# Performance work log

Hardware: AMD Instinct MI355X
Metric: run time of the kernel (lower is better)

The kernel has to match this reference:

```python
import jax, jax.numpy as jnp
import numpy as np

B, TQ, N, E, K = 256, 64, 196, 1024, 512


def setup_inputs() -> dict:
    key = jax.random.key(0)
    ks = jax.random.split(key, 12)
    s_e = 1.0 / np.sqrt(E)
    s_k = 1.0 / np.sqrt(K)
    return {
        "ques_feat": jax.random.normal(ks[0], (B, TQ, E), jnp.float32),
        "img_feat": jax.random.normal(ks[1], (B, E, N), jnp.float32),
        "mask": jnp.ones((B, TQ), jnp.float32),
        # img_corr_dim: Linear(E, E)
        "Wc": jax.random.normal(ks[2], (E, E), jnp.float32) * s_e,
        "bc": jnp.zeros((E,), jnp.float32),
        # ques_embed_dim: Linear(E, K)
        "Wq": jax.random.normal(ks[3], (E, K), jnp.float32) * s_e,
        "bq": jnp.zeros((K,), jnp.float32),
        # img_embed_dim: Linear(E, K)
        "Wi": jax.random.normal(ks[4], (E, K), jnp.float32) * s_e,
        "bi": jnp.zeros((K,), jnp.float32),
        # ques_atten_embedding: Linear(K, 1)
        "wqa": jax.random.normal(ks[5], (K,), jnp.float32) * s_k,
        "bqa": jnp.zeros((), jnp.float32),
        # img_atten_embedding: Linear(K, 1)
        "wia": jax.random.normal(ks[6], (K,), jnp.float32) * s_k,
        "bia": jnp.zeros((), jnp.float32),
    }


def reference(ques_feat, img_feat, mask, Wc, bc, Wq, bq, Wi, bi, wqa, bqa, wia, bia):
    # img_feat: [B, E, N] -> work in [B, N, E] layout
    img_t = jnp.swapaxes(img_feat, 1, 2)                      # [B, N, E]
    img_corr = img_t @ Wc + bc                                # [B, N, E]
    # affinity matrix: tanh(Q @ C^T) -> [B, Tq, N]
    weight = jnp.tanh(jnp.einsum("bqe,bne->bqn", ques_feat, img_corr))
    ques_embed = ques_feat @ Wq + bq                          # [B, Tq, K]
    img_embed = img_t @ Wi + bi                               # [B, N, K]
    # image attention branch
    transform_ques = jnp.einsum("bqk,bqn->bnk", ques_embed, weight)  # [B, N, K]
    img_h = jnp.tanh(transform_ques + img_embed)              # [B, N, K] (dropout p=0)
    img_score = img_h @ wia + bia                             # [B, N]
    img_atten = jax.nn.softmax(img_score, axis=-1)            # [B, N]
    # question attention branch
    transform_img = jnp.einsum("bnk,bqn->bqk", img_embed, weight)    # [B, Tq, K]
    ques_h = jnp.tanh(transform_img + ques_embed)             # [B, Tq, K]
    ques_score = (ques_h @ wqa + bqa) * mask                  # [B, Tq]
    ques_atten = jax.nn.softmax(ques_score, axis=-1)          # [B, Tq]
    # attended features
    ques_atten_feat = jnp.einsum("bq,bqe->be", ques_atten, ques_feat)  # [B, E]
    img_atten_feat = jnp.einsum("bn,bne->be", img_atten, img_t)        # [B, E]
    return ques_atten_feat, img_atten_feat
```

## Files before the change

kernel.cpp:

```cpp
#include <hip/hip_runtime.h>
#include <math.h>


typedef float f32x4 __attribute__((ext_vector_type(4)));
typedef short bf16x8 __attribute__((ext_vector_type(8)));
typedef unsigned short u16;

__device__ __forceinline__ float fast_tanh(float x) {
    float ax = fabsf(x);
    float e  = __expf(-2.0f * ax);
    float r  = (1.0f - e) / (1.0f + e);
    return copysignf(r, x);
}
__device__ __forceinline__ u16 f2bf(float f) {
    unsigned u = __float_as_uint(f);
    u += 0x7FFF + ((u >> 16) & 1);
    return (u16)(u >> 16);
}
__device__ __forceinline__ void split_hl(float f, u16 &h, u16 &l) {
    h = f2bf(f);
    float fh = __uint_as_float((unsigned)h << 16);
    l = f2bf(f - fh);
}
__device__ __forceinline__ void gload_lds16(const u16* g, u16* l) {
    __builtin_amdgcn_global_load_lds(
        (const __attribute__((address_space(1))) unsigned int*)(const void*)g,
        (__attribute__((address_space(3))) unsigned int*)(void*)l, 16, 0, 0);
}

__global__ __launch_bounds__(256) void transpose_split_kernel(
    const float* __restrict__ in, u16* __restrict__ oh, u16* __restrict__ ol,
    const int R, const int C, const long inB, const long outB)
{
    __shared__ float tile[64][65];
    const int t = threadIdx.x;
    const int c0 = blockIdx.x * 64;
    const int r0 = blockIdx.y * 64;
    const long bz = blockIdx.z;
    const float* ib = in + bz * inB;

    #pragma unroll
    for (int i = 0; i < 16; ++i) {
        int idx = i * 256 + t;
        int rl = idx >> 6, cl = idx & 63;
        float v = 0.f;
        if (c0 + cl < C) v = ib[(size_t)(r0 + rl) * C + c0 + cl];
        tile[rl][cl] = v;
    }
    __syncthreads();
    #pragma unroll
    for (int i = 0; i < 16; ++i) {
        int idx = i * 256 + t;
        int cl = idx >> 6, rl = idx & 63;
        if (c0 + cl < C) {
            float v = tile[rl][cl];
            u16 h, l;
            split_hl(v, h, l);
            size_t o = bz * outB + (size_t)(c0 + cl) * R + r0 + rl;
            oh[o] = h; ol[o] = l;
        }
    }
}

__global__ __launch_bounds__(256) void split_flat_kernel(
    const float* __restrict__ in, u16* __restrict__ oh, u16* __restrict__ ol,
    const int n4)
{
    for (int i = blockIdx.x * 256 + threadIdx.x; i < n4; i += gridDim.x * 256) {
        float4 v = ((const float4*)in)[i];
        u16 h0,h1,h2,h3, l0,l1,l2,l3;
        split_hl(v.x,h0,l0); split_hl(v.y,h1,l1);
        split_hl(v.z,h2,l2); split_hl(v.w,h3,l3);
        ((ushort4*)oh)[i] = make_ushort4(h0,h1,h2,h3);
        ((ushort4*)ol)[i] = make_ushort4(l0,l1,l2,l3);
    }
}

template<int WM, int WN, int OUTMODE, bool BATCHED>
__global__ __launch_bounds__(WM*WN*64) void bf_gemm(
    const u16* __restrict__ Ah, const u16* __restrict__ Al,
    const u16* __restrict__ Bh, const u16* __restrict__ Bl,
    const float* __restrict__ bias,
    float* __restrict__ Cf, u16* __restrict__ Ch, u16* __restrict__ Cl,
    const int M, const int N, const int K,
    const int aB, const int bB, const long cB, const int ldc)
{
    constexpr int NW = WM * WN;
    constexpr int AP = WM * 4;
    constexpr int BP = WN * 4;
    constexpr int TOT = (AP + BP) * 2;
    __shared__ __align__(16) u16 smem[(AP + BP) * 2 * 512];

    const int t  = threadIdx.x;
    const int wid = t >> 6, l = t & 63;
    const int wm = wid / WN, wn = wid % WN;
    const int n0 = blockIdx.x * (WN * 64);
    const int m0 = blockIdx.y * (WM * 64);
    const int bz = BATCHED ? blockIdx.z : 0;

    f32x4 acc[4][4];
    #pragma unroll
    for (int p = 0; p < 4; ++p)
        #pragma unroll
        for (int q = 0; q < 4; ++q)
            acc[p][q] = (f32x4){0.f, 0.f, 0.f, 0.f};

    const int lk = (l >> 4) << 3;
    const int lr = l & 15;

    for (int k0 = 0; k0 < K; k0 += 32) {
        #pragma unroll
        for (int j = wid; j < TOT; j += NW) {
            if (j < 2 * AP) {
                int plane = j / AP, p = j % AP;
                int gm = m0 + p * 16 + lr; gm = min(gm, M - 1);
                const u16* src = plane ? Al : Ah;
                const u16* g = src + (BATCHED ? (size_t)bz * aB : 0)
                             + (size_t)gm * K + k0 + lk;
                gload_lds16(g, smem + (plane * AP + p) * 512);
            } else {
                int jj = j - 2 * AP;
                int plane = jj / BP, p = jj % BP;
                int gn = n0 + p * 16 + lr; gn = min(gn, N - 1);
                const u16* src = plane ? Bl : Bh;
                const u16* g = src + (BATCHED ? (size_t)bz * bB : 0)
                             + (size_t)gn * K + k0 + lk;
                gload_lds16(g, smem + (2 * AP + plane * BP + p) * 512);
            }
        }
        __syncthreads();

        bf16x8 a_h[4], a_l[4], b_h[4], b_l[4];
        #pragma unroll
        for (int p = 0; p < 4; ++p) {
            const u16* pa = smem + (wm * 4 + p) * 512 + l * 8;
            a_h[p] = *(const bf16x8*)pa;
            a_l[p] = *(const bf16x8*)(pa + AP * 512);
        }
        #pragma unroll
        for (int q = 0; q < 4; ++q) {
            const u16* pb = smem + (2 * AP + wn * 4 + q) * 512 + l * 8;
            b_h[q] = *(const bf16x8*)pb;
            b_l[q] = *(const bf16x8*)(pb + BP * 512);
        }
        #pragma unroll
        for (int p = 0; p < 4; ++p)
            #pragma unroll
            for (int q = 0; q < 4; ++q)
                acc[p][q] = __builtin_amdgcn_mfma_f32_16x16x32_bf16(a_h[p], b_h[q], acc[p][q], 0, 0, 0);
        #pragma unroll
        for (int p = 0; p < 4; ++p)
            #pragma unroll
            for (int q = 0; q < 4; ++q)
                acc[p][q] = __builtin_amdgcn_mfma_f32_16x16x32_bf16(a_h[p], b_l[q], acc[p][q], 0, 0, 0);
        #pragma unroll
        for (int p = 0; p < 4; ++p)
            #pragma unroll
            for (int q = 0; q < 4; ++q)
                acc[p][q] = __builtin_amdgcn_mfma_f32_16x16x32_bf16(a_l[p], b_h[q], acc[p][q], 0, 0, 0);
        __syncthreads();
    }

    const int colp = l & 15;
    const int rquad = (l >> 4) * 4;
    #pragma unroll
    for (int q = 0; q < 4; ++q) {
        int col = n0 + wn * 64 + q * 16 + colp;
        if (col >= N) continue;
        float bv = bias ? bias[col] : 0.f;
        #pragma unroll
        for (int p = 0; p < 4; ++p) {
            #pragma unroll
            for (int i = 0; i < 4; ++i) {
                int row = m0 + wm * 64 + p * 16 + rquad + i;
                if (row >= M) continue;
                float v = acc[p][q][i] + bv;
                size_t ci = (BATCHED ? (size_t)bz * cB : 0) + (size_t)row * ldc + col;
                if (OUTMODE == 0) {
                    Cf[ci] = v;
                } else if (OUTMODE == 1) {
                    Cf[ci] = fast_tanh(v);
                } else {
                    u16 h, lo2;
                    split_hl(v, h, lo2);
                    Ch[ci] = h; Cl[ci] = lo2;
                }
            }
        }
    }
}

template<int BM,int BN,int BK,int TM,int TN,int ALOAD,int BLOAD,int NBF,int ACT,bool BATCHED>
__global__ __launch_bounds__(256) void gemm_k(
    const float* __restrict__ A, const float* __restrict__ Bm,
    const float* __restrict__ bias, const float* __restrict__ Dadd,
    float* __restrict__ C,
    const int M, const int Nn, const int K,
    const int ab, const int am, const int ak,
    const int bb, const int bk, const int bn,
    const int cb, const int cm)
{
    static_assert(BK == 16, "staging math assumes BK==16");
    __shared__ __align__(16) float As[BK][BM + 4];
    __shared__ __align__(16) float Bs[BK][BN + 4];

    const int t  = threadIdx.x;
    const int n0 = blockIdx.x * BN;
    const int m0 = blockIdx.y * BM;
    const int bz = BATCHED ? blockIdx.z : 0;
    const int w  = t >> 6;
    const int l  = t & 63;
    const int tx = l & 7, ty = l >> 3;
    const int mloc = (w >> 1) * (BM / 2) + ty * TM;
    const int nloc = (w & 1)  * (BN / 2) + tx * TN;

    float acc[TM][TN];
    #pragma unroll
    for (int i = 0; i < TM; ++i)
        #pragma unroll
        for (int j = 0; j < TN; ++j) acc[i][j] = 0.f;

    for (int k0 = 0; k0 < K; k0 += BK) {
        if (ALOAD == 0) {
            constexpr int NF4 = (BM * BK) / (4 * 256);
            #pragma unroll
            for (int i = 0; i < NF4; ++i) {
                int f4i = i * 256 + t;
                int row = f4i >> 2;
                int kq  = (f4i & 3) << 2;
                int gm = m0 + row, gk = k0 + kq;
                float4 v = make_float4(0.f, 0.f, 0.f, 0.f);
                if (gm < M) {
                    int br, r;
                    if (BATCHED)      { br = bz; r = gm; }
                    else if (NBF > 0) { br = gm / NBF; r = gm - br * NBF; }
                    else              { br = 0;  r = gm; }
                    const float* p = A + (size_t)br * ab + (size_t)r * am + gk;
                    if (gk + 4 <= K) v = *(const float4*)p;
                    else {
                        float tv[4] = {0.f, 0.f, 0.f, 0.f};
                        #pragma unroll
                        for (int j = 0; j < 4; ++j) if (gk + j < K) tv[j] = p[j];
                        v = make_float4(tv[0], tv[1], tv[2], tv[3]);
                    }
                }
                As[kq + 0][row] = v.x; As[kq + 1][row] = v.y;
                As[kq + 2][row] = v.z; As[kq + 3][row] = v.w;
            }
        } else {
            constexpr int NF4 = (BM * BK) / (4 * 256);
            #pragma unroll
            for (int i = 0; i < NF4; ++i) {
                int f4i = i * 256 + t;
                int m4 = f4i % (BM / 4);
                int kk = f4i / (BM / 4);
                int gm = m0 + m4 * 4, gk = k0 + kk;
                float4 v = make_float4(0.f, 0.f, 0.f, 0.f);
                if (gm < M && gk < K) {
                    int br, r;
                    if (BATCHED)      { br = bz; r = gm; }
                    else if (NBF > 0) { br = gm / NBF; r = gm - br * NBF; }
                    else              { br = 0;  r = gm; }
                    const float* p = A + (size_t)br * ab + (size_t)r + (size_t)gk * ak;
                    v = *(const float4*)p;
                }
                *(float4*)&As[kk][m4 * 4] = v;
            }
        }
        if (BLOAD == 0) {
            constexpr int NF4 = (BK * BN) / (4 * 256);
            #pragma unroll
            for (int i = 0; i < NF4; ++i) {
                int f4i = i * 256 + t;
                int nq2 = f4i % (BN / 4);
                int kk = f4i / (BN / 4);
                int gn = n0 + nq2 * 4, gk = k0 + kk;
                float4 v = make_float4(0.f, 0.f, 0.f, 0.f);
                if (gk < K && gn + 4 <= Nn) {
                    const float* p = Bm + (size_t)bz * bb + (size_t)gk * bk + gn;
                    v = *(const float4*)p;
                }
                *(float4*)&Bs[kk][nq2 * 4] = v;
            }
        } else {
            constexpr int NF4 = (BK * BN) / (4 * 256);
            #pragma unroll
            for (int i = 0; i < NF4; ++i) {
                int f4i = i * 256 + t;
                int col = f4i >> 2;
                int kq  = (f4i & 3) << 2;
                int gn = n0 + col, gk = k0 + kq;
                float4 v = make_float4(0.f, 0.f, 0.f, 0.f);
                if (gn < Nn) {
                    const float* p = Bm + (size_t)bz * bb + (size_t)gn * bn + gk;
                    if (gk + 4 <= K) v = *(const float4*)p;
                    else {
                        float tv[4] = {0.f, 0.f, 0.f, 0.f};
                        #pragma unroll
                        for (int j = 0; j < 4; ++j) if (gk + j < K) tv[j] = p[j];
                        v = make_float4(tv[0], tv[1], tv[2], tv[3]);
                    }
                }
                Bs[kq + 0][col] = v.x; Bs[kq + 1][col] = v.y;
                Bs[kq + 2][col] = v.z; Bs[kq + 3][col] = v.w;
            }
        }
        __syncthreads();
        #pragma unroll
        for (int kk = 0; kk < BK; ++kk) {
            float a[TM], b[TN];
            #pragma unroll
            for (int i = 0; i < TM; i += 4)
                *(float4*)&a[i] = *(const float4*)&As[kk][mloc + i];
            #pragma unroll
            for (int j = 0; j < TN; j += 4)
                *(float4*)&b[j] = *(const float4*)&Bs[kk][nloc + j];
            #pragma unroll
            for (int i = 0; i < TM; ++i)
                #pragma unroll
                for (int j = 0; j < TN; ++j)
                    acc[i][j] = fmaf(a[i], b[j], acc[i][j]);
        }
        __syncthreads();
    }
    #pragma unroll
    for (int i = 0; i < TM; ++i) {
        int gm = m0 + mloc + i;
        if (gm >= M) continue;
        int br, r;
        if (BATCHED)      { br = bz; r = gm; }
        else if (NBF > 0) { br = gm / NBF; r = gm - br * NBF; }
        else              { br = 0;  r = gm; }
        const size_t crow = (size_t)br * cb + (size_t)r * cm;
        #pragma unroll
        for (int j = 0; j < TN; ++j) {
            int gn = n0 + nloc + j;
            if (gn >= Nn) continue;
            float v = acc[i][j];
            if (bias) v += bias[gn];
            size_t ci = crow + gn;
            if (Dadd) v += Dadd[ci];
            if (ACT == 1) v = fast_tanh(v);
            C[ci] = v;
        }
    }
}

__global__ __launch_bounds__(256) void img_branch_kernel(
    const float* __restrict__ ih,
    const float* __restrict__ wia, const float* __restrict__ bia,
    const float* __restrict__ img_feat,
    float* __restrict__ out)
{
    const int b = blockIdx.x;
    const int t = threadIdx.x;
    const int w = t >> 6, l = t & 63;
    __shared__ float s_w[512];
    __shared__ __align__(16) float sc[200];
    __shared__ float red[8];

    for (int i = t; i < 512; i += 256) s_w[i] = wia[i];
    __syncthreads();

    const float* ihb = ih + (size_t)b * 196 * 512;
    for (int n = w; n < 196; n += 4) {
        const float* row = ihb + n * 512;
        float p = 0.f;
        for (int k = l; k < 512; k += 64) p = fmaf(s_w[k], row[k], p);
        #pragma unroll
        for (int off = 32; off > 0; off >>= 1) p += __shfl_xor(p, off);
        if (l == 0) sc[n] = p + bia[0];
    }
    __syncthreads();

    float v = (t < 196) ? sc[t] : -3.402823466e38f;
    float m = v;
    #pragma unroll
    for (int off = 32; off > 0; off >>= 1) m = fmaxf(m, __shfl_xor(m, off));
    if (l == 0) red[w] = m;
    __syncthreads();
    if (t == 0) {
        float mm = red[0];
        for (int i = 1; i < 4; ++i) mm = fmaxf(mm, red[i]);
        red[4] = mm;
    }
    __syncthreads();
    float mx = red[4];
    float e = (t < 196) ? __expf(v - mx) : 0.f;
    float s = e;
    #pragma unroll
    for (int off = 32; off > 0; off >>= 1) s += __shfl_xor(s, off);
    if (l == 0) red[w] = s;
    __syncthreads();
    if (t == 0) red[5] = 1.f / (red[0] + red[1] + red[2] + red[3]);
    __syncthreads();
    if (t < 196) sc[t] = e * red[5];
    __syncthreads();

    const float* ifb = img_feat + (size_t)b * 1024 * 196;
    for (int e0 = t; e0 < 1024; e0 += 256) {
        const float4* row = (const float4*)(ifb + (size_t)e0 * 196);
        float acc = 0.f;
        #pragma unroll 7
        for (int n4 = 0; n4 < 49; ++n4) {
            float4 x = row[n4];
            float4 a = *(const float4*)&sc[n4 * 4];
            acc = fmaf(x.x, a.x, acc);
            acc = fmaf(x.y, a.y, acc);
            acc = fmaf(x.z, a.z, acc);
            acc = fmaf(x.w, a.w, acc);
        }
        out[(size_t)b * 1024 + e0] = acc;
    }
}

__global__ __launch_bounds__(256) void ques_branch_kernel(
    const float* __restrict__ qh,
    const float* __restrict__ wqa, const float* __restrict__ bqa,
    const float* __restrict__ mask,
    const float* __restrict__ qf,
    float* __restrict__ out)
{
    const int b = blockIdx.x;
    const int t = threadIdx.x;
    const int w = t >> 6, l = t & 63;
    __shared__ float s_w[512];
    __shared__ float sq[64];

    for (int i = t; i < 512; i += 256) s_w[i] = wqa[i];
    __syncthreads();

    const float* qhb = qh + (size_t)b * 64 * 512;
    for (int q = w; q < 64; q += 4) {
        const float* row = qhb + q * 512;
        float p = 0.f;
        for (int k = l; k < 512; k += 64) p = fmaf(s_w[k], row[k], p);
        #pragma unroll
        for (int off = 32; off > 0; off >>= 1) p += __shfl_xor(p, off);
        if (l == 0) sq[q] = (p + bqa[0]) * mask[b * 64 + q];
    }
    __syncthreads();

    if (w == 0) {
        float v = sq[l];
        float m = v;
        #pragma unroll
        for (int off = 32; off > 0; off >>= 1) m = fmaxf(m, __shfl_xor(m, off));
        float e = __expf(v - m);
        float s = e;
        #pragma unroll
        for (int off = 32; off > 0; off >>= 1) s += __shfl_xor(s, off);
        sq[l] = e / s;
    }
    __syncthreads();

    const float* qfb = qf + (size_t)b * 64 * 1024;
    float4 acc = make_float4(0.f, 0.f, 0.f, 0.f);
    for (int q = 0; q < 64; ++q) {
        float a = sq[q];
        float4 x = *(const float4*)(qfb + q * 1024 + t * 4);
        acc.x = fmaf(a, x.x, acc.x);
        acc.y = fmaf(a, x.y, acc.y);
        acc.z = fmaf(a, x.z, acc.z);
        acc.w = fmaf(a, x.w, acc.w);
    }
    *(float4*)(out + (size_t)b * 1024 + t * 4) = acc;
}

extern "C" void kernel_launch(void* const* d_in, const int* in_sizes, int n_in,
                              void* d_out, int out_size, void* d_ws, size_t ws_size,
                              hipStream_t stream) {
    const float* qf  = (const float*)d_in[0];
    const float* imf = (const float*)d_in[1];
    const float* msk = (const float*)d_in[2];
    const float* Wc  = (const float*)d_in[3];
    const float* bc  = (const float*)d_in[4];
    const float* Wq  = (const float*)d_in[5];
    const float* bq  = (const float*)d_in[6];
    const float* Wi  = (const float*)d_in[7];
    const float* bi  = (const float*)d_in[8];
    const float* wqa = (const float*)d_in[9];
    const float* bqa = (const float*)d_in[10];
    const float* wia = (const float*)d_in[11];
    const float* bia = (const float*)d_in[12];
    float* out = (float*)d_out;

    auto cdiv = [](int a, int b) { return (a + b - 1) / b; };

    const size_t perBatch = 802816ull  + 262144ull
                          + 802816ull  + 131072ull
                          + 401408ull  + 50176ull  + 131072ull ;
    const size_t fixedB = 8ull * 1024 * 1024 + 65536;
    int CB = 256;
    while (CB > 1 && fixedB + (size_t)CB * perBatch > ws_size) CB >>= 1;

    char* cur = (char*)d_ws;
    auto carve = [&](size_t bytes) {
        char* p = cur;
        cur += (bytes + 255) & ~255ull;
        return p;
    };
    u16* WcT_h = (u16*)carve(1024ull*1024*2);
    u16* WcT_l = (u16*)carve(1024ull*1024*2);
    u16* WqT_h = (u16*)carve(512ull*1024*2);
    u16* WqT_l = (u16*)carve(512ull*1024*2);
    u16* WiT_h = (u16*)carve(512ull*1024*2);
    u16* WiT_l = (u16*)carve(512ull*1024*2);
    u16* At_h  = (u16*)carve((size_t)CB*196*1024*2);
    u16* At_l  = (u16*)carve((size_t)CB*196*1024*2);
    u16* qf_h  = (u16*)carve((size_t)CB*64*1024*2);
    u16* qf_l  = (u16*)carve((size_t)CB*64*1024*2);
    u16* ic_h  = (u16*)carve((size_t)CB*196*1024*2);
    u16* ic_l  = (u16*)carve((size_t)CB*196*1024*2);
    float* qe  = (float*)carve((size_t)CB*64*512*4);
    float* ie  = (float*)carve((size_t)CB*196*512*4);
    float* wt  = (float*)carve((size_t)CB*64*196*4);
    float* qh  = (float*)carve((size_t)CB*64*512*4);
    float* img_h = (float*)ic_h;

    dim3 blk(256);

    hipLaunchKernelGGL(transpose_split_kernel, dim3(16,16,1), blk, 0, stream,
        Wc, WcT_h, WcT_l, 1024, 1024, 0, 0);
    hipLaunchKernelGGL(transpose_split_kernel, dim3(8,16,1), blk, 0, stream,
        Wq, WqT_h, WqT_l, 1024, 512, 0, 0);
    hipLaunchKernelGGL(transpose_split_kernel, dim3(8,16,1), blk, 0, stream,
        Wi, WiT_h, WiT_l, 1024, 512, 0, 0);

    for (int c0 = 0; c0 < 256; c0 += CB) {
        const float* qfc  = qf  + (size_t)c0 * 65536;
        const float* imfc = imf + (size_t)c0 * 200704;
        const float* mskc = msk + (size_t)c0 * 64;
        float* outq = out + (size_t)c0 * 1024;
        float* outi = out + 262144 + (size_t)c0 * 1024;

        hipLaunchKernelGGL(transpose_split_kernel, dim3(4,16,CB), blk, 0, stream,
            imfc, At_h, At_l, 1024, 196, 200704, 200704);
        {
            int n4 = CB * 16384;
            hipLaunchKernelGGL(split_flat_kernel, dim3(min(2048, cdiv(n4,256))), blk, 0, stream,
                qfc, qf_h, qf_l, n4);
        }

        hipLaunchKernelGGL((bf_gemm<2,2,0,false>), dim3(4, cdiv(CB*64,128), 1), blk, 0, stream,
            qf_h, qf_l, WqT_h, WqT_l, bq, qe, (u16*)nullptr, (u16*)nullptr,
            CB*64, 512, 1024, 0, 0, 0, 512);

        hipLaunchKernelGGL((bf_gemm<2,2,2,false>), dim3(8, cdiv(CB*196,128), 1), blk, 0, stream,
            At_h, At_l, WcT_h, WcT_l, bc, (float*)nullptr, ic_h, ic_l,
            CB*196, 1024, 1024, 0, 0, 0, 1024);

        hipLaunchKernelGGL((bf_gemm<2,2,0,false>), dim3(4, cdiv(CB*196,128), 1), blk, 0, stream,
            At_h, At_l, WiT_h, WiT_l, bi, ie, (u16*)nullptr, (u16*)nullptr,
            CB*196, 512, 1024, 0, 0, 0, 512);

        hipLaunchKernelGGL((bf_gemm<1,2,1,true>), dim3(2, 1, CB), dim3(128), 0, stream,
            qf_h, qf_l, ic_h, ic_l, (const float*)nullptr, wt, (u16*)nullptr, (u16*)nullptr,
            64, 196, 1024, 65536, 200704, 12544, 196);

        hipLaunchKernelGGL((gemm_k<128,128,16,8,8,1,0,0,1,true>),
            dim3(4, 2, CB), blk, 0, stream,
            wt, qe, (const float*)nullptr, ie, img_h,
            196, 512, 64,  12544,1,196,  32768,512,1,  100352,512);

        hipLaunchKernelGGL(img_branch_kernel, dim3(CB), blk, 0, stream,
            img_h, wia, bia, imfc, outi);

        hipLaunchKernelGGL((gemm_k<64,64,16,4,4,0,0,0,1,true>),
            dim3(8, 1, CB), blk, 0, stream,
            wt, ie, (const float*)nullptr, qe, qh,
            64, 512, 196,  12544,196,1,  100352,512,1,  32768,512);

        hipLaunchKernelGGL(ques_branch_kernel, dim3(CB), blk, 0, stream,
            qh, wqa, bqa, mskc, qfc, outq);
    }
}
```

Baseline: 1.765 ms.

## Double-buffer LDS staging in bf_gemm and add XCD-aware block swizzle

The split-bf16 MFMA GEMM now stages the next K-slice into a second LDS buffer while the current slice is being computed. It uses an explicit vmcnt wait and raw barriers in place of a full __syncthreads before each compute step. It also adds an optional workgroup-ID remap that spreads consecutive blocks across eight chunks, aiming for better L2 locality across XCDs on the non-batched GEMMs. The cost is doubled LDS per block, which may reduce occupancy, and reliance on hand-tuned waitcnt counts for correctness.

```diff
diff --git a/kernel.cpp b/kernel.cpp
--- a/kernel.cpp
+++ b/kernel.cpp
@@ -76,7 +76,7 @@
     }
 }
 
-template<int WM, int WN, int OUTMODE, bool BATCHED>
+template<int WM, int WN, int OUTMODE, bool BATCHED, bool SWZ>
 __global__ __launch_bounds__(WM*WN*64) void bf_gemm(
     const u16* __restrict__ Ah, const u16* __restrict__ Al,
     const u16* __restrict__ Bh, const u16* __restrict__ Bl,
@@ -85,17 +85,30 @@
     const int M, const int N, const int K,
     const int aB, const int bB, const long cB, const int ldc)
 {
-    constexpr int NW = WM * WN;
-    constexpr int AP = WM * 4;
-    constexpr int BP = WN * 4;
-    constexpr int TOT = (AP + BP) * 2;
-    __shared__ __align__(16) u16 smem[(AP + BP) * 2 * 512];
+    constexpr int NW  = WM * WN;
+    constexpr int AP  = WM * 4;
+    constexpr int BP  = WN * 4;
+    constexpr int PAN = (AP + BP) * 2;
+    constexpr int JPW = PAN / NW;
+    __shared__ __align__(16) u16 smem[2 * PAN * 512];
 
     const int t  = threadIdx.x;
     const int wid = t >> 6, l = t & 63;
     const int wm = wid / WN, wn = wid % WN;
-    const int n0 = blockIdx.x * (WN * 64);
-    const int m0 = blockIdx.y * (WM * 64);
+
+    int bx, by;
+    if (SWZ) {
+        int nwg = gridDim.x * gridDim.y;
+        int bid = blockIdx.x + gridDim.x * blockIdx.y;
+        if ((nwg & 7) == 0) {
+            int chunk = nwg >> 3;
+            int wg = (bid & 7) * chunk + (bid >> 3);
+            bx = wg % gridDim.x; by = wg / gridDim.x;
+        } else { bx = blockIdx.x; by = blockIdx.y; }
+    } else { bx = blockIdx.x; by = blockIdx.y; }
+
+    const int n0 = bx * (WN * 64);
+    const int m0 = by * (WM * 64);
     const int bz = BATCHED ? blockIdx.z : 0;
 
     f32x4 acc[4][4];
@@ -108,38 +121,50 @@
     const int lk = (l >> 4) << 3;
     const int lr = l & 15;
 
-    for (int k0 = 0; k0 < K; k0 += 32) {
-        #pragma unroll
-        for (int j = wid; j < TOT; j += NW) {
+    auto stage = [&](int k0, int buf) {
+        u16* dst0 = smem + buf * (PAN * 512);
+        #pragma unroll
+        for (int j = wid; j < PAN; j += NW) {
+            const u16* g;
             if (j < 2 * AP) {
                 int plane = j / AP, p = j % AP;
                 int gm = m0 + p * 16 + lr; gm = min(gm, M - 1);
                 const u16* src = plane ? Al : Ah;
-                const u16* g = src + (BATCHED ? (size_t)bz * aB : 0)
-                             + (size_t)gm * K + k0 + lk;
-                gload_lds16(g, smem + (plane * AP + p) * 512);
+                g = src + (BATCHED ? (size_t)bz * aB : 0)
+                  + (size_t)gm * K + k0 + lk;
             } else {
                 int jj = j - 2 * AP;
                 int plane = jj / BP, p = jj % BP;
                 int gn = n0 + p * 16 + lr; gn = min(gn, N - 1);
                 const u16* src = plane ? Bl : Bh;
-                const u16* g = src + (BATCHED ? (size_t)bz * bB : 0)
-                             + (size_t)gn * K + k0 + lk;
-                gload_lds16(g, smem + (2 * AP + plane * BP + p) * 512);
+                g = src + (BATCHED ? (size_t)bz * bB : 0)
+                  + (size_t)gn * K + k0 + lk;
             }
-        }
-        __syncthreads();
-
+            gload_lds16(g, dst0 + j * 512);
+        }
+    };
+
+    const int nk = K >> 5;
+    stage(0, 0);
+    int cur = 0;
+    for (int ks = 0; ks < nk; ++ks) {
+        const bool pf = (ks + 1 < nk);
+        if (pf) stage((ks + 1) << 5, cur ^ 1);
+        if (pf) asm volatile("s_waitcnt vmcnt(%0)" :: "i"(JPW) : "memory");
+        else    asm volatile("s_waitcnt vmcnt(0)" ::: "memory");
+        asm volatile("s_barrier" ::: "memory");
+
+        const u16* sb = smem + cur * (PAN * 512);
         bf16x8 a_h[4], a_l[4], b_h[4], b_l[4];
         #pragma unroll
         for (int p = 0; p < 4; ++p) {
-            const u16* pa = smem + (wm * 4 + p) * 512 + l * 8;
+            const u16* pa = sb + (wm * 4 + p) * 512 + l * 8;
             a_h[p] = *(const bf16x8*)pa;
             a_l[p] = *(const bf16x8*)(pa + AP * 512);
         }
         #pragma unroll
         for (int q = 0; q < 4; ++q) {
-            const u16* pb = smem + (2 * AP + wn * 4 + q) * 512 + l * 8;
+            const u16* pb = sb + (2 * AP + wn * 4 + q) * 512 + l * 8;
             b_h[q] = *(const bf16x8*)pb;
             b_l[q] = *(const bf16x8*)(pb + BP * 512);
         }
@@ -158,7 +183,10 @@
             #pragma unroll
             for (int q = 0; q < 4; ++q)
                 acc[p][q] = __builtin_amdgcn_mfma_f32_16x16x32_bf16(a_l[p], b_h[q], acc[p][q], 0, 0, 0);
-        __syncthreads();
+
+        asm volatile("s_waitcnt lgkmcnt(0)" ::: "memory");
+        asm volatile("s_barrier" ::: "memory");
+        cur ^= 1;
     }
 
     const int colp = l & 15;
@@ -542,19 +570,19 @@
                 qfc, qf_h, qf_l, n4);
         }
 
-        hipLaunchKernelGGL((bf_gemm<2,2,0,false>), dim3(4, cdiv(CB*64,128), 1), blk, 0, stream,
+        hipLaunchKernelGGL((bf_gemm<2,2,0,false,true>), dim3(4, cdiv(CB*64,128), 1), blk, 0, stream,
             qf_h, qf_l, WqT_h, WqT_l, bq, qe, (u16*)nullptr, (u16*)nullptr,
             CB*64, 512, 1024, 0, 0, 0, 512);
 
-        hipLaunchKernelGGL((bf_gemm<2,2,2,false>), dim3(8, cdiv(CB*196,128), 1), blk, 0, stream,
+        hipLaunchKernelGGL((bf_gemm<2,2,2,false,true>), dim3(8, cdiv(CB*196,128), 1), blk, 0, stream,
             At_h, At_l, WcT_h, WcT_l, bc, (float*)nullptr, ic_h, ic_l,
             CB*196, 1024, 1024, 0, 0, 0, 1024);
 
-        hipLaunchKernelGGL((bf_gemm<2,2,0,false>), dim3(4, cdiv(CB*196,128), 1), blk, 0, stream,
+        hipLaunchKernelGGL((bf_gemm<2,2,0,false,true>), dim3(4, cdiv(CB*196,128), 1), blk, 0, stream,
             At_h, At_l, WiT_h, WiT_l, bi, ie, (u16*)nullptr, (u16*)nullptr,
             CB*196, 512, 1024, 0, 0, 0, 512);
 
-        hipLaunchKernelGGL((bf_gemm<1,2,1,true>), dim3(2, 1, CB), dim3(128), 0, stream,
+        hipLaunchKernelGGL((bf_gemm<1,2,1,true,false>), dim3(2, 1, CB), dim3(128), 0, stream,
             qf_h, qf_l, ic_h, ic_l, (const float*)nullptr, wt, (u16*)nullptr, (u16*)nullptr,
             64, 196, 1024, 65536, 200704, 12544, 196);
 
```

New measurement: 3.621 ms. +105.2%, slower.
